# Performance work log

Hardware: AMD Instinct MI355X
Metric: run time of the kernel (lower is better)

Reference implementation:

```python
import jax, jax.numpy as jnp
import numpy as np

D_MODEL = 1024
N_HEAD = 16
N_HEAD_MOE = 8
N_EXPERTS = 8
TOP_N = 2
CAP_FACTOR = 1.25
THRESHOLD = 0.2
BAL_COEF = 0.01
Z_COEF = 0.001
B, S = 8, 1024


def setup_inputs() -> dict:
    key = jax.random.key(0)
    ks = jax.random.split(key, 12)
    d, E = D_MODEL, N_EXPERTS
    w = lambda k, shape: jax.random.normal(k, shape, jnp.float32) * 0.02
    return {
        "x": jax.random.normal(ks[0], (B, S, d), jnp.float32),
        "Wq": w(ks[1], (d, d)), "Wk": w(ks[2], (d, d)), "Wv": w(ks[3], (d, d)), "Wo": w(ks[4], (d, d)),
        "bq": jnp.zeros((d,), jnp.float32), "bk": jnp.zeros((d,), jnp.float32),
        "bv": jnp.zeros((d,), jnp.float32), "bo": jnp.zeros((d,), jnp.float32),
        "ln1_g": jnp.ones((d,), jnp.float32), "ln1_b": jnp.zeros((d,), jnp.float32),
        "ln2_g": jnp.ones((d,), jnp.float32), "ln2_b": jnp.zeros((d,), jnp.float32),
        "gate_W": w(ks[5], (d, E)),
        "eWq": w(ks[6], (E, d, d)), "eWk": w(ks[7], (E, d, d)),
        "eWv": w(ks[8], (E, d, d)), "eWo": w(ks[9], (E, d, d)),
    }


def _layernorm(x, g, b, eps=1e-5):
    mu = jnp.mean(x, -1, keepdims=True)
    var = jnp.var(x, -1, keepdims=True)
    return (x - mu) * jax.lax.rsqrt(var + eps) * g + b


def _mha(x, Wq, Wk, Wv, bq, bk, bv, Wo, bo):
    b, s, d = x.shape
    h, hd = N_HEAD, d // N_HEAD
    q = (x @ Wq + bq).reshape(b, s, h, hd)
    k = (x @ Wk + bk).reshape(b, s, h, hd)
    v = (x @ Wv + bv).reshape(b, s, h, hd)
    att = jax.nn.softmax(jnp.einsum('bqhd,bkhd->bhqk', q, k) * (hd ** -0.5), axis=-1)
    o = jnp.einsum('bhqk,bkhd->bqhd', att, v).reshape(b, s, d)
    return o @ Wo + bo


def _moe(x, gate_W, eWq, eWk, eWv, eWo):
    # ST-MoE style top-n routing with capacity dropping; experts are self-attention blocks.
    b, s, d = x.shape
    E = N_EXPERTS
    C = int(S * TOP_N * CAP_FACTOR / E)  # per-expert capacity (per batch row)
    logits = x @ gate_W                      # [b,s,E]
    z_loss = jnp.mean(jnp.square(jax.nn.logsumexp(logits, axis=-1)))
    probs = jax.nn.softmax(logits, axis=-1)
    gates, idxs = jax.lax.top_k(probs, TOP_N)  # [b,s,TOP_N]
    # load-balance loss: E * sum_e (top-1 dispatch fraction) * (mean router prob)
    f = jnp.mean(jax.nn.one_hot(idxs[..., 0], E, dtype=x.dtype), axis=(0, 1))
    P = jnp.mean(probs, axis=(0, 1))
    balance_loss = E * jnp.sum(f * P)

    bb = jnp.broadcast_to(jnp.arange(b)[:, None], (b, s))
    counts = jnp.zeros((b, E), jnp.int32)
    expert_in = jnp.zeros((E, b, C, d), x.dtype)
    slots = []
    for k in range(TOP_N):  # small fixed loop over routing slots
        e_idx = idxs[..., k]
        g = gates[..., k]
        keep_thr = (g > THRESHOLD) if k > 0 else jnp.ones(g.shape, dtype=bool)
        oh = jax.nn.one_hot(e_idx, E, dtype=jnp.int32) * keep_thr[..., None].astype(jnp.int32)
        # exclusive running position within each (batch, expert) buffer
        pos_all = jnp.cumsum(oh, axis=1) - oh + counts[:, None, :]
        pos = jnp.take_along_axis(pos_all, e_idx[..., None], axis=2)[..., 0]
        counts = counts + jnp.sum(oh, axis=1)
        keep = keep_thr & (pos < C)
        p = jnp.clip(pos, 0, C - 1)
        expert_in = expert_in.at[e_idx, bb, p].add(x * keep[..., None].astype(x.dtype))
        slots.append((e_idx, p, keep, g))

    # each expert: multi-head self-attention over its C capacity slots
    h, hd = N_HEAD_MOE, d // N_HEAD_MOE
    q = jnp.einsum('ebcd,edf->ebcf', expert_in, eWq).reshape(E, b, C, h, hd)
    kk = jnp.einsum('ebcd,edf->ebcf', expert_in, eWk).reshape(E, b, C, h, hd)
    v = jnp.einsum('ebcd,edf->ebcf', expert_in, eWv).reshape(E, b, C, h, hd)
    att = jax.nn.softmax(jnp.einsum('ebqhd,ebkhd->ebhqk', q, kk) * (hd ** -0.5), axis=-1)
    o = jnp.einsum('ebhqk,ebkhd->ebqhd', att, v).reshape(E, b, C, d)
    expert_out = jnp.einsum('ebcd,edf->ebcf', o, eWo)

    # combine: gather each token's slot output, weighted by its gate
    y = jnp.zeros_like(x)
    for e_idx, p, keep, g in slots:
        y = y + expert_out[e_idx, bb, p] * (g * keep.astype(x.dtype))[..., None]
    bal = BAL_COEF * balance_loss
    zl = Z_COEF * z_loss
    return y, bal + zl, bal, zl


def reference(x, Wq, Wk, Wv, Wo, bq, bk, bv, bo, ln1_g, ln1_b, ln2_g, ln2_b,
              gate_W, eWq, eWk, eWv, eWo):
    attn = _mha(x, Wq, Wk, Wv, bq, bk, bv, Wo, bo)
    x1 = _layernorm(x + attn, ln1_g, ln1_b)
    moe_out, aux, bal, zl = _moe(x1, gate_W, eWq, eWk, eWv, eWo)
    out = _layernorm(x1 + moe_out, ln2_g, ln2_b)
    return (out, aux, bal, zl)
```

## Files before the change

kernel.cpp:

```cpp
#include <hip/hip_runtime.h>
#include <hip/hip_bf16.h>
#include <math.h>

#define DM    1024
#define NH1   16
#define HDIM1 64
#define NH2   8
#define HDIM2 128
#define NE    8
#define CAPE  320
#define BATCH 8
#define SEQ   1024
#define NTOK  (BATCH*SEQ)
#define OUTN  ((long)NTOK*DM)
#define ECB   ((long)BATCH*CAPE*DM)

typedef short bf16x8 __attribute__((ext_vector_type(8)));
typedef float f32x4  __attribute__((ext_vector_type(4)));

__device__ __forceinline__ unsigned short f2bf(float f) {
    __hip_bfloat16 h = __float2bfloat16(f);
    return *reinterpret_cast<unsigned short*>(&h);
}
__device__ __forceinline__ float bf2f(unsigned short u) {
    unsigned int x = ((unsigned int)u) << 16;
    return __builtin_bit_cast(float, x);
}

__device__ __forceinline__ void async16(const void* g, void* lds) {
    __builtin_amdgcn_global_load_lds(
        (const __attribute__((address_space(1))) unsigned int*)g,
        (__attribute__((address_space(3))) unsigned int*)lds, 16, 0, 0);
}

__device__ __forceinline__ void gemm_core(
    const unsigned short* __restrict__ A, const unsigned short* __restrict__ Bt,
    int m0, int n0, int K, short* ldsA, short* ldsB, f32x4 (&acc)[4][4])
{
    const int t    = threadIdx.x;
    const int lane = t & 63, w = t >> 6;
    const int wr = w >> 1, wc = w & 1;
    const int lq = lane >> 4, lm = lane & 15;
    const int srow = w*16 + (lane >> 2);
    const int skc  = (lane & 3) * 8;
    for (int kb = 0; kb < K; kb += 32) {
        #pragma unroll
        for (int p = 0; p < 2; ++p) {
            async16(A  + (size_t)(m0 + srow + p*64)*K + kb + skc,
                    &ldsA[(w*16 + p*64)*32]);
            async16(Bt + (size_t)(n0 + srow + p*64)*K + kb + skc,
                    &ldsB[(w*16 + p*64)*32]);
        }
        __syncthreads();
        bf16x8 aF[4], bF[4];
        #pragma unroll
        for (int i = 0; i < 4; ++i)
            aF[i] = *(const bf16x8*)&ldsA[(wr*64 + i*16 + lm)*32 + lq*8];
        #pragma unroll
        for (int j = 0; j < 4; ++j)
            bF[j] = *(const bf16x8*)&ldsB[(wc*64 + j*16 + lm)*32 + lq*8];
        #pragma unroll
        for (int i = 0; i < 4; ++i)
            #pragma unroll
            for (int j = 0; j < 4; ++j)
                acc[i][j] = __builtin_amdgcn_mfma_f32_16x16x32_bf16(aF[i], bF[j], acc[i][j], 0, 0, 0);
        __syncthreads();
    }
}

__global__ __launch_bounds__(256) void gemm_bt_f32(
    const unsigned short* __restrict__ A, const unsigned short* __restrict__ Bt,
    const float* __restrict__ bias, float* __restrict__ C, int N, int K)
{
    __shared__ short ldsA[128*32];
    __shared__ short ldsB[128*32];
    const int lane = threadIdx.x & 63, w = threadIdx.x >> 6;
    const int wr = w >> 1, wc = w & 1;
    const int lq = lane >> 4, lm = lane & 15;
    const int m0 = blockIdx.y * 128, n0 = blockIdx.x * 128;
    f32x4 acc[4][4];
    #pragma unroll
    for (int i = 0; i < 4; ++i)
        #pragma unroll
        for (int j = 0; j < 4; ++j) acc[i][j] = (f32x4){0.f,0.f,0.f,0.f};
    gemm_core(A, Bt, m0, n0, K, ldsA, ldsB, acc);
    #pragma unroll
    for (int j = 0; j < 4; ++j) {
        const int gcol = n0 + wc*64 + j*16 + lm;
        const float badd = bias ? bias[gcol] : 0.f;
        #pragma unroll
        for (int i = 0; i < 4; ++i) {
            const int grow = m0 + wr*64 + i*16 + lq*4;
            #pragma unroll
            for (int r = 0; r < 4; ++r)
                C[(size_t)(grow + r)*N + gcol] = acc[i][j][r] + badd;
        }
    }
}

__global__ __launch_bounds__(256) void gemm_qkv(
    const unsigned short* __restrict__ A, const unsigned short* __restrict__ Bt,
    const float* __restrict__ bq, const float* __restrict__ bk, const float* __restrict__ bv,
    unsigned short* __restrict__ C)
{
    __shared__ short ldsA[128*32];
    __shared__ short ldsB[128*32];
    const int lane = threadIdx.x & 63, w = threadIdx.x >> 6;
    const int wr = w >> 1, wc = w & 1;
    const int lq = lane >> 4, lm = lane & 15;
    const int m0 = blockIdx.y * 128, n0g = blockIdx.x * 128;
    const int buf = n0g >> 10;
    const float* bias = (buf == 0) ? bq : (buf == 1) ? bk : bv;
    unsigned short* Cb = C + (size_t)buf * OUTN;
    f32x4 acc[4][4];
    #pragma unroll
    for (int i = 0; i < 4; ++i)
        #pragma unroll
        for (int j = 0; j < 4; ++j) acc[i][j] = (f32x4){0.f,0.f,0.f,0.f};
    gemm_core(A, Bt, m0, n0g, DM, ldsA, ldsB, acc);
    #pragma unroll
    for (int j = 0; j < 4; ++j) {
        const int gcol = (n0g & 1023) + wc*64 + j*16 + lm;
        const float badd = bias[gcol];
        #pragma unroll
        for (int i = 0; i < 4; ++i) {
            const int grow = m0 + wr*64 + i*16 + lq*4;
            #pragma unroll
            for (int r = 0; r < 4; ++r)
                Cb[(size_t)(grow + r)*DM + gcol] = f2bf(acc[i][j][r] + badd);
        }
    }
}

__global__ __launch_bounds__(256) void gemm_eqkv(
    const unsigned short* __restrict__ A,
    const unsigned short* __restrict__ eWTq, const unsigned short* __restrict__ eWTk,
    const unsigned short* __restrict__ eWTv,
    unsigned short* __restrict__ Cq, unsigned short* __restrict__ Ck,
    unsigned short* __restrict__ Cv, int ebase)
{
    __shared__ short ldsA[128*32];
    __shared__ short ldsB[128*32];
    const int lane = threadIdx.x & 63, w = threadIdx.x >> 6;
    const int wr = w >> 1, wc = w & 1;
    const int lq = lane >> 4, lm = lane & 15;
    const int z = blockIdx.z;
    const int eloc = blockIdx.y / 20;
    const unsigned short* Bt =
        ((z == 0) ? eWTq : (z == 1) ? eWTk : eWTv) + (size_t)(ebase + eloc) * (1024l*1024l);
    unsigned short* C = (z == 0) ? Cq : (z == 1) ? Ck : Cv;
    const int m0 = blockIdx.y * 128, n0 = blockIdx.x * 128;
    f32x4 acc[4][4];
    #pragma unroll
    for (int i = 0; i < 4; ++i)
        #pragma unroll
        for (int j = 0; j < 4; ++j) acc[i][j] = (f32x4){0.f,0.f,0.f,0.f};
    gemm_core(A, Bt, m0, n0, DM, ldsA, ldsB, acc);
    #pragma unroll
    for (int j = 0; j < 4; ++j) {
        const int gcol = n0 + wc*64 + j*16 + lm;
        #pragma unroll
        for (int i = 0; i < 4; ++i) {
            const int grow = m0 + wr*64 + i*16 + lq*4;
            #pragma unroll
            for (int r = 0; r < 4; ++r)
                C[(size_t)(grow + r)*DM + gcol] = f2bf(acc[i][j][r]);
        }
    }
}

__global__ __launch_bounds__(256) void gemm_eout(
    const unsigned short* __restrict__ A, const unsigned short* __restrict__ eWTo,
    unsigned short* __restrict__ C, int ebase)
{
    __shared__ short ldsA[128*32];
    __shared__ short ldsB[128*32];
    const int lane = threadIdx.x & 63, w = threadIdx.x >> 6;
    const int wr = w >> 1, wc = w & 1;
    const int lq = lane >> 4, lm = lane & 15;
    const int eloc = blockIdx.y / 20;
    const unsigned short* Bt = eWTo + (size_t)(ebase + eloc) * (1024l*1024l);
    const int m0 = blockIdx.y * 128, n0 = blockIdx.x * 128;
    f32x4 acc[4][4];
    #pragma unroll
    for (int i = 0; i < 4; ++i)
        #pragma unroll
        for (int j = 0; j < 4; ++j) acc[i][j] = (f32x4){0.f,0.f,0.f,0.f};
    gemm_core(A, Bt, m0, n0, DM, ldsA, ldsB, acc);
    #pragma unroll
    for (int j = 0; j < 4; ++j) {
        const int gcol = n0 + wc*64 + j*16 + lm;
        #pragma unroll
        for (int i = 0; i < 4; ++i) {
            const int grow = m0 + wr*64 + i*16 + lq*4;
            #pragma unroll
            for (int r = 0; r < 4; ++r)
                C[(size_t)(grow + r)*DM + gcol] = f2bf(acc[i][j][r]);
        }
    }
}

template<int HD, int NS>
__global__ __launch_bounds__(256) void flash_mfma(
    const unsigned short* __restrict__ Q, const unsigned short* __restrict__ K,
    const unsigned short* __restrict__ V, unsigned short* __restrict__ O,
    int rows, float scale)
{
    constexpr int KT = 64;
    constexpr int PADQ = HD + 8;
    constexpr int NKT = HD / 32;
    constexpr int NDT = HD / 16;
    constexpr int CG  = HD / 8;
    constexpr int RPR = 256 / CG;
    constexpr int NP  = KT / RPR;
    constexpr int PST = 76;
    __shared__ __align__(16) unsigned short ks[KT * PADQ];
    __shared__ __align__(16) unsigned short vt[HD * KT];
    __shared__ __align__(16) unsigned short pP[4][16 * PST];
    const int t = threadIdx.x, lane = t & 63, w = t >> 6;
    const int lm = lane & 15, quad = lane >> 4;
    const int q0 = blockIdx.x * (64 * NS);
    const long base = (long)blockIdx.z * rows * DM + (long)blockIdx.y * HD;
    const int srow = t / CG, scg = t % CG;

    bf16x8 aQ[NS][NKT];
    #pragma unroll
    for (int s = 0; s < NS; ++s) {
        if (s) __syncthreads();
        #pragma unroll
        for (int r = 0; r < 64 / RPR; ++r) {
            int row = srow + r * RPR;
            *(bf16x8*)&ks[row * PADQ + scg * 8] =
                *(const bf16x8*)&Q[base + (long)(q0 + s * 64 + row) * DM + scg * 8];
        }
        __syncthreads();
        #pragma unroll
        for (int kk = 0; kk < NKT; ++kk)
            aQ[s][kk] = *(const bf16x8*)&ks[(w * 16 + lm) * PADQ + kk * 32 + quad * 8];
    }

    float m4[NS][4], l4[NS][4];
    f32x4 aco[NS][NDT];
    #pragma unroll
    for (int s = 0; s < NS; ++s) {
        #pragma unroll
        for (int r = 0; r < 4; ++r) { m4[s][r] = -1e30f; l4[s][r] = 0.f; }
        #pragma unroll
        for (int d = 0; d < NDT; ++d) aco[s][d] = (f32x4){0.f,0.f,0.f,0.f};
    }

    bf16x8 kr[NP], vr[NP];
    #pragma unroll
    for (int r = 0; r < NP; ++r) {
        int row = srow + r * RPR;
        kr[r] = *(const bf16x8*)&K[base + (long)row * DM + scg * 8];
        vr[r] = *(const bf16x8*)&V[base + (long)row * DM + scg * 8];
    }

    for (int k0 = 0; k0 < rows; k0 += KT) {
        __syncthreads();
        #pragma unroll
        for (int r = 0; r < NP; ++r) {
            int row = srow + r * RPR;
            *(bf16x8*)&ks[row * PADQ + scg * 8] = kr[r];
            #pragma unroll
            for (int u = 0; u < 8; ++u) {
                int d = scg * 8 + u;
                vt[d * KT + ((((row >> 3) ^ (d >> 3) ^ d) & 7)) * 8 + (row & 7)] = ((short*)&vr[r])[u];
            }
        }
        __syncthreads();
        if (k0 + KT < rows) {
            #pragma unroll
            for (int r = 0; r < NP; ++r) {
                int row = srow + r * RPR;
                kr[r] = *(const bf16x8*)&K[base + (long)(k0 + KT + row) * DM + scg * 8];
                vr[r] = *(const bf16x8*)&V[base + (long)(k0 + KT + row) * DM + scg * 8];
            }
        }
        #pragma unroll
        for (int s = 0; s < NS; ++s) {
            f32x4 sc[4];
            #pragma unroll
            for (int n = 0; n < 4; ++n) {
                f32x4 c = (f32x4){0.f,0.f,0.f,0.f};
                #pragma unroll
                for (int kk = 0; kk < NKT; ++kk) {
                    bf16x8 bK = *(const bf16x8*)&ks[(n * 16 + lm) * PADQ + kk * 32 + quad * 8];
                    c = __builtin_amdgcn_mfma_f32_16x16x32_bf16(aQ[s][kk], bK, c, 0, 0, 0);
                }
                #pragma unroll
                for (int r = 0; r < 4; ++r) c[r] *= scale;
                sc[n] = c;
            }
            float alpha[4];
            #pragma unroll
            for (int r = 0; r < 4; ++r) {
                float mx = fmaxf(fmaxf(sc[0][r], sc[1][r]), fmaxf(sc[2][r], sc[3][r]));
                #pragma unroll
                for (int off = 1; off < 16; off <<= 1)
                    mx = fmaxf(mx, __shfl_xor(mx, off, 64));
                float mnew = fmaxf(m4[s][r], mx);
                alpha[r] = __expf(m4[s][r] - mnew);
                m4[s][r] = mnew;
                float sum = 0.f;
                #pragma unroll
                for (int n = 0; n < 4; ++n) {
                    float p = __expf(sc[n][r] - mnew);
                    sc[n][r] = p; sum += p;
                }
                #pragma unroll
                for (int off = 1; off < 16; off <<= 1)
                    sum += __shfl_xor(sum, off, 64);
                l4[s][r] = l4[s][r] * alpha[r] + sum;
            }
            #pragma unroll
            for (int n = 0; n < 4; ++n)
                #pragma unroll
                for (int r = 0; r < 4; ++r)
                    pP[w][(quad * 4 + r) * PST + n * 16 + lm] = f2bf(sc[n][r]);
            #pragma unroll
            for (int d = 0; d < NDT; ++d)
                #pragma unroll
                for (int r = 0; r < 4; ++r) aco[s][d][r] *= alpha[r];
            #pragma unroll
            for (int d = 0; d < NDT; ++d) {
                #pragma unroll
                for (int kk = 0; kk < 2; ++kk) {
                    bf16x8 aP = *(const bf16x8*)&pP[w][lm * PST + kk * 32 + quad * 8];
                    int dd = d * 16 + lm;
                    int jb = kk * 4 + quad;
                    bf16x8 bV = *(const bf16x8*)&vt[dd * KT + (((jb ^ (dd >> 3) ^ dd) & 7) * 8)];
                    aco[s][d] = __builtin_amdgcn_mfma_f32_16x16x32_bf16(aP, bV, aco[s][d], 0, 0, 0);
                }
            }
        }
    }
    #pragma unroll
    for (int s = 0; s < NS; ++s)
        #pragma unroll
        for (int r = 0; r < 4; ++r) {
            float inv = 1.f / l4[s][r];
            #pragma unroll
            for (int d = 0; d < NDT; ++d)
                O[base + (long)(q0 + s * 64 + w * 16 + quad * 4 + r) * DM + d * 16 + lm] =
                    f2bf(aco[s][d][r] * inv);
        }
}

__global__ __launch_bounds__(256) void transpose_bf16(
    const float* __restrict__ src, unsigned short* __restrict__ dst)
{
    __shared__ float tile[32][33];
    const long mb = (long)blockIdx.z * (1024l*1024l);
    const int tx = threadIdx.x & 31, ty = threadIdx.x >> 5;
    const int r0 = blockIdx.y * 32, c0 = blockIdx.x * 32;
    #pragma unroll
    for (int rr = ty; rr < 32; rr += 8)
        tile[rr][tx] = src[mb + (long)(r0+rr)*1024 + c0 + tx];
    __syncthreads();
    #pragma unroll
    for (int rr = ty; rr < 32; rr += 8)
        dst[mb + (long)(c0+rr)*1024 + r0 + tx] = f2bf(tile[tx][rr]);
}

__global__ __launch_bounds__(256) void convert_bf16(
    const float* __restrict__ src, unsigned short* __restrict__ dst, long n)
{
    long i = ((long)blockIdx.x*256 + threadIdx.x)*4;
    if (i >= n) return;
    float4 v = *(const float4*)&src[i];
    ushort4 o = { f2bf(v.x), f2bf(v.y), f2bf(v.z), f2bf(v.w) };
    *(ushort4*)&dst[i] = o;
}

__global__ __launch_bounds__(256) void ln_residual(
    const float* __restrict__ X, const float* __restrict__ R,
    const float* __restrict__ gam, const float* __restrict__ bet,
    float* __restrict__ Y)
{
    const long row = blockIdx.x;
    const int t = threadIdx.x;
    float4 xv = *(const float4*)&X[row*DM + t*4];
    float4 rv = *(const float4*)&R[row*DM + t*4];
    float v0=xv.x+rv.x, v1=xv.y+rv.y, v2=xv.z+rv.z, v3=xv.w+rv.w;
    float s  = v0+v1+v2+v3;
    float s2 = v0*v0+v1*v1+v2*v2+v3*v3;
    #pragma unroll
    for (int off = 32; off > 0; off >>= 1) {
        s  += __shfl_down(s,  off, 64);
        s2 += __shfl_down(s2, off, 64);
    }
    __shared__ float red[8];
    __shared__ float mv[2];
    const int wid = t >> 6;
    if ((t & 63) == 0) { red[wid] = s; red[4+wid] = s2; }
    __syncthreads();
    if (t == 0) {
        float S  = red[0]+red[1]+red[2]+red[3];
        float S2 = red[4]+red[5]+red[6]+red[7];
        float mean = S * (1.f/DM);
        float var  = S2 * (1.f/DM) - mean*mean;
        mv[0] = mean; mv[1] = rsqrtf(var + 1e-5f);
    }
    __syncthreads();
    float mean = mv[0], inv = mv[1];
    float4 g4 = *(const float4*)&gam[t*4];
    float4 b4 = *(const float4*)&bet[t*4];
    float4 o4;
    o4.x = (v0-mean)*inv*g4.x + b4.x;
    o4.y = (v1-mean)*inv*g4.y + b4.y;
    o4.z = (v2-mean)*inv*g4.z + b4.z;
    o4.w = (v3-mean)*inv*g4.w + b4.w;
    *(float4*)&Y[row*DM + t*4] = o4;
}

__global__ __launch_bounds__(256) void combine_ln(
    const float* __restrict__ X1, const unsigned short* __restrict__ Eout,
    const int* __restrict__ e1, const int* __restrict__ pos1,
    const int* __restrict__ keep1, const float* __restrict__ g1,
    const int* __restrict__ e2, const int* __restrict__ pos2,
    const int* __restrict__ keep2, const float* __restrict__ g2,
    const float* __restrict__ gam, const float* __restrict__ bet,
    float* __restrict__ Y)
{
    const long row = blockIdx.x;
    const int b = (int)(row >> 10);
    const int t = threadIdx.x;
    float4 xv = *(const float4*)&X1[row*DM + t*4];
    float v0=xv.x, v1=xv.y, v2=xv.z, v3=xv.w;
    const float w1 = keep1[row] ? g1[row] : 0.f;
    const float w2 = keep2[row] ? g2[row] : 0.f;
    if (w1 != 0.f) {
        ushort4 u = *(const ushort4*)&Eout[(((size_t)e1[row]*BATCH + b)*CAPE + pos1[row])*DM + t*4];
        v0 += w1*bf2f(u.x); v1 += w1*bf2f(u.y); v2 += w1*bf2f(u.z); v3 += w1*bf2f(u.w);
    }
    if (w2 != 0.f) {
        ushort4 u = *(const ushort4*)&Eout[(((size_t)e2[row]*BATCH + b)*CAPE + pos2[row])*DM + t*4];
        v0 += w2*bf2f(u.x); v1 += w2*bf2f(u.y); v2 += w2*bf2f(u.z); v3 += w2*bf2f(u.w);
    }
    float s  = v0+v1+v2+v3;
    float s2 = v0*v0+v1*v1+v2*v2+v3*v3;
    #pragma unroll
    for (int off = 32; off > 0; off >>= 1) {
        s  += __shfl_down(s,  off, 64);
        s2 += __shfl_down(s2, off, 64);
    }
    __shared__ float red[8];
    __shared__ float mv[2];
    const int wid = t >> 6;
    if ((t & 63) == 0) { red[wid] = s; red[4+wid] = s2; }
    __syncthreads();
    if (t == 0) {
        float S  = red[0]+red[1]+red[2]+red[3];
        float S2 = red[4]+red[5]+red[6]+red[7];
        float mean = S * (1.f/DM);
        float var  = S2 * (1.f/DM) - mean*mean;
        mv[0] = mean; mv[1] = rsqrtf(var + 1e-5f);
    }
    __syncthreads();
    float mean = mv[0], inv = mv[1];
    float4 g4 = *(const float4*)&gam[t*4];
    float4 b4 = *(const float4*)&bet[t*4];
    float4 o4;
    o4.x = (v0-mean)*inv*g4.x + b4.x;
    o4.y = (v1-mean)*inv*g4.y + b4.y;
    o4.z = (v2-mean)*inv*g4.z + b4.z;
    o4.w = (v3-mean)*inv*g4.w + b4.w;
    *(float4*)&Y[row*DM + t*4] = o4;
}

__global__ __launch_bounds__(256) void gate_kernel(
    const float* __restrict__ X1, const float* __restrict__ gW,
    int* __restrict__ e1, int* __restrict__ e2,
    float* __restrict__ g1, float* __restrict__ g2,
    float* __restrict__ accum)
{
    const int t = threadIdx.x, l = t & 63, w = t >> 6;
    const int gwave = blockIdx.x * 4 + w;
    float zacc = 0.f, pacc[8], facc[8];
    #pragma unroll
    for (int e = 0; e < 8; ++e) { pacc[e] = 0.f; facc[e] = 0.f; }

    for (int tok = gwave; tok < NTOK; tok += 2048) {
        const float* xr = X1 + (long)tok*DM;
        float part[8];
        #pragma unroll
        for (int e = 0; e < 8; ++e) part[e] = 0.f;
        #pragma unroll
        for (int pass = 0; pass < 4; ++pass) {
            const int i0 = pass*256 + l*4;
            float4 xv = *(const float4*)&xr[i0];
            const float xs[4] = {xv.x, xv.y, xv.z, xv.w};
            #pragma unroll
            for (int u = 0; u < 4; ++u) {
                float4 w0 = *(const float4*)&gW[(i0+u)*8];
                float4 w1 = *(const float4*)&gW[(i0+u)*8+4];
                part[0]+=xs[u]*w0.x; part[1]+=xs[u]*w0.y; part[2]+=xs[u]*w0.z; part[3]+=xs[u]*w0.w;
                part[4]+=xs[u]*w1.x; part[5]+=xs[u]*w1.y; part[6]+=xs[u]*w1.z; part[7]+=xs[u]*w1.w;
            }
        }
        #pragma unroll
        for (int e = 0; e < 8; ++e) {
            float v = part[e];
            #pragma unroll
            for (int off = 32; off > 0; off >>= 1) v += __shfl_down(v, off, 64);
            part[e] = v;
        }
        if (l == 0) {
            float mx = part[0];
            #pragma unroll
            for (int e = 1; e < 8; ++e) mx = fmaxf(mx, part[e]);
            float p[8]; float sum = 0.f;
            #pragma unroll
            for (int e = 0; e < 8; ++e) { p[e] = __expf(part[e]-mx); sum += p[e]; }
            float lse = mx + __logf(sum);
            float isum = 1.f/sum;
            #pragma unroll
            for (int e = 0; e < 8; ++e) { p[e] *= isum; pacc[e] += p[e]; }
            int b1 = 0;
            #pragma unroll
            for (int e = 1; e < 8; ++e) if (p[e] > p[b1]) b1 = e;
            int b2 = (b1 == 0) ? 1 : 0;
            #pragma unroll
            for (int e = 0; e < 8; ++e) if (e != b1 && e != b2 && p[e] > p[b2]) b2 = e;
            e1[tok] = b1; e2[tok] = b2; g1[tok] = p[b1]; g2[tok] = p[b2];
            zacc += lse*lse;
            facc[b1] += 1.f;
        }
    }
    __shared__ float red[4][17];
    if (l == 0) {
        red[w][0] = zacc;
        #pragma unroll
        for (int e = 0; e < 8; ++e) { red[w][1+e] = pacc[e]; red[w][9+e] = facc[e]; }
    }
    __syncthreads();
    if (t < 17)
        atomicAdd(&accum[t], red[0][t] + red[1][t] + red[2][t] + red[3][t]);
}

__global__ __launch_bounds__(64) void route_scan(
    const int* __restrict__ e1, const int* __restrict__ e2,
    const float* __restrict__ g2,
    int* __restrict__ pos1, int* __restrict__ keep1,
    int* __restrict__ pos2, int* __restrict__ keep2,
    int* __restrict__ slotmap)
{
    const int b = blockIdx.x;
    const int l = threadIdx.x;
    __shared__ int cnt[8];
    if (l < 8) cnt[l] = 0;
    __syncthreads();
    for (int slot = 0; slot < 2; ++slot) {
        const int* eArr = slot ? e2 : e1;
        for (int c = 0; c < SEQ/64; ++c) {
            const int tk = b*SEQ + c*64 + l;
            const int e = eArr[tk];
            const bool valid = slot ? (g2[tk] > 0.2f) : true;
            unsigned long long mymask = 0ull; int addmine = 0;
            #pragma unroll
            for (int ee = 0; ee < 8; ++ee) {
                unsigned long long bm = __ballot(valid && (e == ee));
                if (e == ee) mymask = bm;
                if (l == ee) addmine = (int)__popcll(bm);
            }
            const int p  = cnt[e] + (int)__popcll(mymask & ((1ull << l) - 1ull));
            const int kp = (valid && p < CAPE) ? 1 : 0;
            const int pc = p < CAPE ? p : (CAPE-1);
            if (slot == 0) { pos1[tk] = pc; keep1[tk] = kp; }
            else           { pos2[tk] = pc; keep2[tk] = kp; }
            if (kp) slotmap[(e*BATCH + b)*CAPE + pc] = tk;
            __syncthreads();
            if (l < 8) cnt[l] += addmine;
            __syncthreads();
        }
    }
}

__global__ __launch_bounds__(256) void gather_chunk(
    const float* __restrict__ X1, const int* __restrict__ slotmap,
    unsigned short* __restrict__ Ein, int ebase)
{
    const int slot = blockIdx.x;
    const int t = threadIdx.x;
    const int tok = slotmap[ebase*(BATCH*CAPE) + slot];
    float4 v4 = make_float4(0.f, 0.f, 0.f, 0.f);
    if (tok >= 0) v4 = *(const float4*)&X1[(long)tok*DM + t*4];
    ushort4 o = { f2bf(v4.x), f2bf(v4.y), f2bf(v4.z), f2bf(v4.w) };
    *(ushort4*)&Ein[(long)slot*DM + t*4] = o;
}

__global__ void finalize_loss(const float* __restrict__ accum, float* __restrict__ out)
{
    float z = accum[0] * (1.0f/NTOK);
    float s = 0.f;
    for (int e = 0; e < 8; ++e)
        s += (accum[1+e] * (1.0f/NTOK)) * (accum[9+e] * (1.0f/NTOK));
    float bal = 0.01f * 8.0f * s;
    float zl  = 0.001f * z;
    out[OUTN]   = bal + zl;
    out[OUTN+1] = bal;
    out[OUTN+2] = zl;
}

extern "C" void kernel_launch(void* const* d_in, const int* in_sizes, int n_in,
                              void* d_out, int out_size, void* d_ws, size_t ws_size,
                              hipStream_t stream)
{
    (void)in_sizes; (void)n_in; (void)out_size; (void)ws_size;
    const float* x    = (const float*)d_in[0];
    const float* Wq   = (const float*)d_in[1];
    const float* Wk   = (const float*)d_in[2];
    const float* Wv   = (const float*)d_in[3];
    const float* Wo   = (const float*)d_in[4];
    const float* bq   = (const float*)d_in[5];
    const float* bk   = (const float*)d_in[6];
    const float* bv   = (const float*)d_in[7];
    const float* bo   = (const float*)d_in[8];
    const float* ln1g = (const float*)d_in[9];
    const float* ln1b = (const float*)d_in[10];
    const float* ln2g = (const float*)d_in[11];
    const float* ln2b = (const float*)d_in[12];
    const float* gW   = (const float*)d_in[13];
    const float* eWq  = (const float*)d_in[14];
    const float* eWk  = (const float*)d_in[15];
    const float* eWv  = (const float*)d_in[16];
    const float* eWo  = (const float*)d_in[17];
    float* out = (float*)d_out;

    char* ws = (char*)d_ws;
    const size_t MB = 1048576;
    const long MATE = 1024l*1024l;
    unsigned short* WTq  = (unsigned short*)(ws);
    unsigned short* WTk  = WTq + 1*MATE;
    unsigned short* WTv  = WTq + 2*MATE;
    unsigned short* WTo  = WTq + 3*MATE;
    unsigned short* eWTq = WTq + 4*MATE;
    unsigned short* eWTk = WTq + 12*MATE;
    unsigned short* eWTv = WTq + 20*MATE;
    unsigned short* eWTo = WTq + 28*MATE;
    int*   e1i   = (int*)(ws + 72*MB);
    int*   e2i   = e1i + NTOK;
    int*   pos1  = e1i + 2*NTOK;
    int*   pos2  = e1i + 3*NTOK;
    int*   keep1 = e1i + 4*NTOK;
    int*   keep2 = e1i + 5*NTOK;
    int*   slotmap = e1i + 6*NTOK;
    float* g1f   = (float*)(e1i + 6*NTOK + NE*BATCH*CAPE);
    float* g2f   = g1f + NTOK;
    float* accum = g2f + NTOK;
    unsigned short* xb = (unsigned short*)(ws + 74*MB);
    unsigned short* ob = (unsigned short*)(ws + 90*MB);
    unsigned short* Qb = (unsigned short*)(ws + 106*MB);
    float* Pf = (float*)(ws + 106*MB);
    float* x1 = (float*)(ws + 154*MB);
    unsigned short* eoutAll = (unsigned short*)(ws + 74*MB);
    unsigned short* Einb = (unsigned short*)(ws + 114*MB);
    unsigned short* eqb  = (unsigned short*)(ws + 124*MB);
    unsigned short* ekb  = (unsigned short*)(ws + 134*MB);
    unsigned short* evb  = (unsigned short*)(ws + 144*MB);
    unsigned short* eob  = Einb;

    dim3 blk(256);
    dim3 tgrid(32, 32, 1), tgrid8(32, 32, 8);

    transpose_bf16<<<tgrid,  blk, 0, stream>>>(Wq,  WTq);
    transpose_bf16<<<tgrid,  blk, 0, stream>>>(Wk,  WTk);
    transpose_bf16<<<tgrid,  blk, 0, stream>>>(Wv,  WTv);
    transpose_bf16<<<tgrid,  blk, 0, stream>>>(Wo,  WTo);
    transpose_bf16<<<tgrid8, blk, 0, stream>>>(eWq, eWTq);
    transpose_bf16<<<tgrid8, blk, 0, stream>>>(eWk, eWTk);
    transpose_bf16<<<tgrid8, blk, 0, stream>>>(eWv, eWTv);
    transpose_bf16<<<tgrid8, blk, 0, stream>>>(eWo, eWTo);
    convert_bf16<<<NTOK, blk, 0, stream>>>(x, xb, OUTN);

    gemm_qkv<<<dim3(3*DM/128, NTOK/128), blk, 0, stream>>>(xb, WTq, bq, bk, bv, Qb);
    flash_mfma<HDIM1,2><<<dim3(SEQ/128, NH1, BATCH), blk, 0, stream>>>(
        Qb, Qb + OUTN, Qb + 2*OUTN, ob, SEQ, 0.125f);
    gemm_bt_f32<<<dim3(DM/128, NTOK/128), blk, 0, stream>>>(ob, WTo, bo, Pf, DM, DM);
    ln_residual<<<NTOK, blk, 0, stream>>>(x, Pf, ln1g, ln1b, x1);

    hipMemsetAsync(accum, 0, 17*sizeof(float), stream);
    hipMemsetAsync(slotmap, 0xFF, NE*BATCH*CAPE*sizeof(int), stream);
    gate_kernel<<<512, blk, 0, stream>>>(x1, gW, e1i, e2i, g1f, g2f, accum);
    route_scan<<<BATCH, dim3(64), 0, stream>>>(e1i, e2i, g2f, pos1, keep1, pos2, keep2, slotmap);

    for (int c = 0; c < 4; ++c) {
        const int ebase = c*2;
        gather_chunk<<<2*BATCH*CAPE, blk, 0, stream>>>(x1, slotmap, Einb, ebase);
        gemm_eqkv<<<dim3(DM/128, 2*BATCH*CAPE/128, 3), blk, 0, stream>>>(
            Einb, eWTq, eWTk, eWTv, eqb, ekb, evb, ebase);
        flash_mfma<HDIM2,1><<<dim3(CAPE/64, NH2, 2*BATCH), blk, 0, stream>>>(
            eqb, ekb, evb, eob, CAPE, 0.088388347648318447f);
        gemm_eout<<<dim3(DM/128, 2*BATCH*CAPE/128), blk, 0, stream>>>(
            eob, eWTo, eoutAll + (size_t)ebase*ECB, ebase);
    }

    combine_ln<<<NTOK, blk, 0, stream>>>(x1, eoutAll, e1i, pos1, keep1, g1f,
                                         e2i, pos2, keep2, g2f, ln2g, ln2b, out);
    finalize_loss<<<1, 1, 0, stream>>>(accum, out);
}
```

Baseline: 1.027 ms.

## Fuse expert token gather into QKV GEMM and process experts in chunks of four

Removes the separate gather kernel by loading slot-mapped bf16 token rows directly inside the expert QKV GEMM, with a zero buffer standing in for empty slots. Experts are processed in two chunks of four instead of four chunks of two, and each chunk's outputs are accumulated into the output buffer before a final in-place layernorm. The first layernorm now also writes a bf16 copy, and the dense attention switches to 64-row query tiles. The new GEMM loop is not double-buffered and the combine adds extra read-modify-write passes over the fp32 output.

```diff
diff --git a/kernel.cpp b/kernel.cpp
--- a/kernel.cpp
+++ b/kernel.cpp
@@ -13,7 +13,6 @@
 #define SEQ   1024
 #define NTOK  (BATCH*SEQ)
 #define OUTN  ((long)NTOK*DM)
-#define ECB   ((long)BATCH*CAPE*DM)
 
 typedef short bf16x8 __attribute__((ext_vector_type(8)));
 typedef float f32x4  __attribute__((ext_vector_type(4)));
@@ -132,8 +131,9 @@
     }
 }
 
-__global__ __launch_bounds__(256) void gemm_eqkv(
-    const unsigned short* __restrict__ A,
+__global__ __launch_bounds__(256) void gemm_eqkv_gather(
+    const unsigned short* __restrict__ X1b, const int* __restrict__ slotmap,
+    const unsigned short* __restrict__ zbuf,
     const unsigned short* __restrict__ eWTq, const unsigned short* __restrict__ eWTk,
     const unsigned short* __restrict__ eWTv,
     unsigned short* __restrict__ Cq, unsigned short* __restrict__ Ck,
@@ -150,12 +150,38 @@
         ((z == 0) ? eWTq : (z == 1) ? eWTk : eWTv) + (size_t)(ebase + eloc) * (1024l*1024l);
     unsigned short* C = (z == 0) ? Cq : (z == 1) ? Ck : Cv;
     const int m0 = blockIdx.y * 128, n0 = blockIdx.x * 128;
+    const int srow = w*16 + (lane >> 2);
+    const int skc  = (lane & 3) * 8;
+    const int sbase = ebase * (BATCH*CAPE);
+    const int t0 = slotmap[sbase + m0 + srow];
+    const int t1 = slotmap[sbase + m0 + srow + 64];
+    const unsigned short* a0 = (t0 >= 0) ? X1b + (size_t)t0 * DM : zbuf;
+    const unsigned short* a1 = (t1 >= 0) ? X1b + (size_t)t1 * DM : zbuf;
     f32x4 acc[4][4];
     #pragma unroll
     for (int i = 0; i < 4; ++i)
         #pragma unroll
         for (int j = 0; j < 4; ++j) acc[i][j] = (f32x4){0.f,0.f,0.f,0.f};
-    gemm_core(A, Bt, m0, n0, DM, ldsA, ldsB, acc);
+    for (int kb = 0; kb < DM; kb += 32) {
+        async16(a0 + kb + skc, &ldsA[(w*16)*32]);
+        async16(a1 + kb + skc, &ldsA[(w*16 + 64)*32]);
+        async16(Bt + (size_t)(n0 + srow)*DM + kb + skc,      &ldsB[(w*16)*32]);
+        async16(Bt + (size_t)(n0 + srow + 64)*DM + kb + skc, &ldsB[(w*16 + 64)*32]);
+        __syncthreads();
+        bf16x8 aF[4], bF[4];
+        #pragma unroll
+        for (int i = 0; i < 4; ++i)
+            aF[i] = *(const bf16x8*)&ldsA[(wr*64 + i*16 + lm)*32 + lq*8];
+        #pragma unroll
+        for (int j = 0; j < 4; ++j)
+            bF[j] = *(const bf16x8*)&ldsB[(wc*64 + j*16 + lm)*32 + lq*8];
+        #pragma unroll
+        for (int i = 0; i < 4; ++i)
+            #pragma unroll
+            for (int j = 0; j < 4; ++j)
+                acc[i][j] = __builtin_amdgcn_mfma_f32_16x16x32_bf16(aF[i], bF[j], acc[i][j], 0, 0, 0);
+        __syncthreads();
+    }
     #pragma unroll
     for (int j = 0; j < 4; ++j) {
         const int gcol = n0 + wc*64 + j*16 + lm;
@@ -377,7 +403,7 @@
 __global__ __launch_bounds__(256) void ln_residual(
     const float* __restrict__ X, const float* __restrict__ R,
     const float* __restrict__ gam, const float* __restrict__ bet,
-    float* __restrict__ Y)
+    float* __restrict__ Yf, unsigned short* __restrict__ Yb)
 {
     const long row = blockIdx.x;
     const int t = threadIdx.x;
@@ -412,33 +438,50 @@
     o4.y = (v1-mean)*inv*g4.y + b4.y;
     o4.z = (v2-mean)*inv*g4.z + b4.z;
     o4.w = (v3-mean)*inv*g4.w + b4.w;
-    *(float4*)&Y[row*DM + t*4] = o4;
-}
-
-__global__ __launch_bounds__(256) void combine_ln(
-    const float* __restrict__ X1, const unsigned short* __restrict__ Eout,
+    *(float4*)&Yf[row*DM + t*4] = o4;
+    ushort4 ub = { f2bf(o4.x), f2bf(o4.y), f2bf(o4.z), f2bf(o4.w) };
+    *(ushort4*)&Yb[row*DM + t*4] = ub;
+}
+
+__global__ __launch_bounds__(256) void accum_chunk(
+    float* __restrict__ out, const unsigned short* __restrict__ Eout,
     const int* __restrict__ e1, const int* __restrict__ pos1,
     const int* __restrict__ keep1, const float* __restrict__ g1,
     const int* __restrict__ e2, const int* __restrict__ pos2,
     const int* __restrict__ keep2, const float* __restrict__ g2,
-    const float* __restrict__ gam, const float* __restrict__ bet,
-    float* __restrict__ Y)
+    int ebase)
 {
     const long row = blockIdx.x;
     const int b = (int)(row >> 10);
     const int t = threadIdx.x;
-    float4 xv = *(const float4*)&X1[row*DM + t*4];
+    const int E1 = e1[row] - ebase;
+    const int E2 = e2[row] - ebase;
+    const bool h1 = (E1 >= 0) && (E1 < 4) && (keep1[row] != 0);
+    const bool h2 = (E2 >= 0) && (E2 < 4) && (keep2[row] != 0);
+    if (!h1 && !h2) return;
+    float4 acc = *(const float4*)&out[row*DM + t*4];
+    if (h1) {
+        const float w1 = g1[row];
+        ushort4 u = *(const ushort4*)&Eout[((size_t)(E1*BATCH + b)*CAPE + pos1[row])*DM + t*4];
+        acc.x += w1*bf2f(u.x); acc.y += w1*bf2f(u.y);
+        acc.z += w1*bf2f(u.z); acc.w += w1*bf2f(u.w);
+    }
+    if (h2) {
+        const float w2 = g2[row];
+        ushort4 u = *(const ushort4*)&Eout[((size_t)(E2*BATCH + b)*CAPE + pos2[row])*DM + t*4];
+        acc.x += w2*bf2f(u.x); acc.y += w2*bf2f(u.y);
+        acc.z += w2*bf2f(u.z); acc.w += w2*bf2f(u.w);
+    }
+    *(float4*)&out[row*DM + t*4] = acc;
+}
+
+__global__ __launch_bounds__(256) void ln_inplace(
+    float* __restrict__ Y, const float* __restrict__ gam, const float* __restrict__ bet)
+{
+    const long row = blockIdx.x;
+    const int t = threadIdx.x;
+    float4 xv = *(const float4*)&Y[row*DM + t*4];
     float v0=xv.x, v1=xv.y, v2=xv.z, v3=xv.w;
-    const float w1 = keep1[row] ? g1[row] : 0.f;
-    const float w2 = keep2[row] ? g2[row] : 0.f;
-    if (w1 != 0.f) {
-        ushort4 u = *(const ushort4*)&Eout[(((size_t)e1[row]*BATCH + b)*CAPE + pos1[row])*DM + t*4];
-        v0 += w1*bf2f(u.x); v1 += w1*bf2f(u.y); v2 += w1*bf2f(u.z); v3 += w1*bf2f(u.w);
-    }
-    if (w2 != 0.f) {
-        ushort4 u = *(const ushort4*)&Eout[(((size_t)e2[row]*BATCH + b)*CAPE + pos2[row])*DM + t*4];
-        v0 += w2*bf2f(u.x); v1 += w2*bf2f(u.y); v2 += w2*bf2f(u.z); v3 += w2*bf2f(u.w);
-    }
     float s  = v0+v1+v2+v3;
     float s2 = v0*v0+v1*v1+v2*v2+v3*v3;
     #pragma unroll
@@ -576,19 +619,6 @@
             __syncthreads();
         }
     }
-}
-
-__global__ __launch_bounds__(256) void gather_chunk(
-    const float* __restrict__ X1, const int* __restrict__ slotmap,
-    unsigned short* __restrict__ Ein, int ebase)
-{
-    const int slot = blockIdx.x;
-    const int t = threadIdx.x;
-    const int tok = slotmap[ebase*(BATCH*CAPE) + slot];
-    float4 v4 = make_float4(0.f, 0.f, 0.f, 0.f);
-    if (tok >= 0) v4 = *(const float4*)&X1[(long)tok*DM + t*4];
-    ushort4 o = { f2bf(v4.x), f2bf(v4.y), f2bf(v4.z), f2bf(v4.w) };
-    *(ushort4*)&Ein[(long)slot*DM + t*4] = o;
 }
 
 __global__ void finalize_loss(const float* __restrict__ accum, float* __restrict__ out)
@@ -650,17 +680,17 @@
     float* g1f   = (float*)(e1i + 6*NTOK + NE*BATCH*CAPE);
     float* g2f   = g1f + NTOK;
     float* accum = g2f + NTOK;
-    unsigned short* xb = (unsigned short*)(ws + 74*MB);
-    unsigned short* ob = (unsigned short*)(ws + 90*MB);
-    unsigned short* Qb = (unsigned short*)(ws + 106*MB);
+    unsigned short* zbuf = (unsigned short*)(ws + 73*MB);
+    unsigned short* xb  = (unsigned short*)(ws + 74*MB);
+    unsigned short* x1b = (unsigned short*)(ws + 74*MB);
+    unsigned short* ob  = (unsigned short*)(ws + 90*MB);
+    unsigned short* Qb  = (unsigned short*)(ws + 106*MB);
     float* Pf = (float*)(ws + 106*MB);
-    float* x1 = (float*)(ws + 154*MB);
-    unsigned short* eoutAll = (unsigned short*)(ws + 74*MB);
-    unsigned short* Einb = (unsigned short*)(ws + 114*MB);
-    unsigned short* eqb  = (unsigned short*)(ws + 124*MB);
-    unsigned short* ekb  = (unsigned short*)(ws + 134*MB);
-    unsigned short* evb  = (unsigned short*)(ws + 144*MB);
-    unsigned short* eob  = Einb;
+    unsigned short* eqb = (unsigned short*)(ws + 90*MB);
+    unsigned short* ekb = (unsigned short*)(ws + 110*MB);
+    unsigned short* evb = (unsigned short*)(ws + 130*MB);
+    unsigned short* eob = (unsigned short*)(ws + 150*MB);
+    unsigned short* eoc = eqb;
 
     dim3 blk(256);
     dim3 tgrid(32, 32, 1), tgrid8(32, 32, 8);
@@ -676,28 +706,29 @@
     convert_bf16<<<NTOK, blk, 0, stream>>>(x, xb, OUTN);
 
     gemm_qkv<<<dim3(3*DM/128, NTOK/128), blk, 0, stream>>>(xb, WTq, bq, bk, bv, Qb);
-    flash_mfma<HDIM1,2><<<dim3(SEQ/128, NH1, BATCH), blk, 0, stream>>>(
+    flash_mfma<HDIM1,1><<<dim3(SEQ/64, NH1, BATCH), blk, 0, stream>>>(
         Qb, Qb + OUTN, Qb + 2*OUTN, ob, SEQ, 0.125f);
     gemm_bt_f32<<<dim3(DM/128, NTOK/128), blk, 0, stream>>>(ob, WTo, bo, Pf, DM, DM);
-    ln_residual<<<NTOK, blk, 0, stream>>>(x, Pf, ln1g, ln1b, x1);
+    ln_residual<<<NTOK, blk, 0, stream>>>(x, Pf, ln1g, ln1b, out, x1b);
 
     hipMemsetAsync(accum, 0, 17*sizeof(float), stream);
     hipMemsetAsync(slotmap, 0xFF, NE*BATCH*CAPE*sizeof(int), stream);
-    gate_kernel<<<512, blk, 0, stream>>>(x1, gW, e1i, e2i, g1f, g2f, accum);
+    hipMemsetAsync(zbuf, 0, 4096, stream);
+    gate_kernel<<<512, blk, 0, stream>>>(out, gW, e1i, e2i, g1f, g2f, accum);
     route_scan<<<BATCH, dim3(64), 0, stream>>>(e1i, e2i, g2f, pos1, keep1, pos2, keep2, slotmap);
 
-    for (int c = 0; c < 4; ++c) {
-        const int ebase = c*2;
-        gather_chunk<<<2*BATCH*CAPE, blk, 0, stream>>>(x1, slotmap, Einb, ebase);
-        gemm_eqkv<<<dim3(DM/128, 2*BATCH*CAPE/128, 3), blk, 0, stream>>>(
-            Einb, eWTq, eWTk, eWTv, eqb, ekb, evb, ebase);
-        flash_mfma<HDIM2,1><<<dim3(CAPE/64, NH2, 2*BATCH), blk, 0, stream>>>(
+    for (int c = 0; c < 2; ++c) {
+        const int ebase = c*4;
+        gemm_eqkv_gather<<<dim3(DM/128, 4*BATCH*CAPE/128, 3), blk, 0, stream>>>(
+            x1b, slotmap, zbuf, eWTq, eWTk, eWTv, eqb, ekb, evb, ebase);
+        flash_mfma<HDIM2,1><<<dim3(CAPE/64, NH2, 4*BATCH), blk, 0, stream>>>(
             eqb, ekb, evb, eob, CAPE, 0.088388347648318447f);
-        gemm_eout<<<dim3(DM/128, 2*BATCH*CAPE/128), blk, 0, stream>>>(
-            eob, eWTo, eoutAll + (size_t)ebase*ECB, ebase);
-    }
-
-    combine_ln<<<NTOK, blk, 0, stream>>>(x1, eoutAll, e1i, pos1, keep1, g1f,
-                                         e2i, pos2, keep2, g2f, ln2g, ln2b, out);
+        gemm_eout<<<dim3(DM/128, 4*BATCH*CAPE/128), blk, 0, stream>>>(
+            eob, eWTo, eoc, ebase);
+        accum_chunk<<<NTOK, blk, 0, stream>>>(out, eoc, e1i, pos1, keep1, g1f,
+                                              e2i, pos2, keep2, g2f, ebase);
+    }
+
+    ln_inplace<<<NTOK, blk, 0, stream>>>(out, ln2g, ln2b);
     finalize_loss<<<1, 1, 0, stream>>>(accum, out);
 }
```

Result: faster. 917.0 us (-10.7%).
